# Performance work log

Hardware: AMD Instinct MI355X
Metric: run time of the kernel (lower is better)

The kernel has to match this reference:

```python
import jax, jax.numpy as jnp
import numpy as np

N_NODES = 100000
N_EDGES = 1600000
D_IN = 64
D_OUT = 64
BN_EPS = 1e-5


def setup_inputs() -> dict:
    key = jax.random.key(0)
    ks = jax.random.split(key, 8)
    x = jax.random.normal(ks[0], (N_NODES, D_IN), dtype=jnp.float32)
    edge_index = jax.random.randint(ks[1], (2, N_EDGES), 0, N_NODES, dtype=jnp.int64)
    s_e = 1.0 / np.sqrt(2 * D_IN)
    s_n = 1.0 / np.sqrt(D_IN + D_OUT)
    W_edge = jax.random.uniform(ks[2], (2 * D_IN, D_OUT), jnp.float32, -s_e, s_e)
    b_edge = jax.random.uniform(ks[3], (D_OUT,), jnp.float32, -s_e, s_e)
    W_node = jax.random.uniform(ks[4], (D_IN + D_OUT, D_OUT), jnp.float32, -s_n, s_n)
    b_node = jax.random.uniform(ks[5], (D_OUT,), jnp.float32, -s_n, s_n)
    prelu_a = jnp.asarray(0.25, dtype=jnp.float32)  # nn.PReLU default single slope
    bn_gamma = jnp.ones((D_OUT,), dtype=jnp.float32)
    bn_beta = jnp.zeros((D_OUT,), dtype=jnp.float32)
    return {"x": x, "edge_index": edge_index, "W_edge": W_edge, "b_edge": b_edge,
            "W_node": W_node, "b_node": b_node, "prelu_a": prelu_a,
            "bn_gamma": bn_gamma, "bn_beta": bn_beta}


def reference(x, edge_index, W_edge, b_edge, W_node, b_node, prelu_a, bn_gamma, bn_beta):
    src, dst = edge_index[0], edge_index[1]
    # edge model: message from concat(source, target) node features  [E, 2*D_IN]
    msg_in = jnp.concatenate([x[src], x[dst]], axis=-1)
    msg = msg_in @ W_edge + b_edge                              # [E, D_OUT]
    # scatter-sum aggregate messages at destination nodes       [N, D_OUT]
    agg = jax.ops.segment_sum(msg, dst, num_segments=N_NODES)
    # node model
    h = jnp.concatenate([x, agg], axis=-1) @ W_node + b_node    # [N, D_OUT]
    # PReLU (single shared slope)
    h = jnp.where(h >= 0, h, prelu_a * h)
    # BatchNorm over nodes (training-mode batch stats, biased variance)
    mean = jnp.mean(h, axis=0)
    var = jnp.mean(jnp.square(h - mean), axis=0)
    h = (h - mean) * jax.lax.rsqrt(var + BN_EPS) * bn_gamma + bn_beta
    return h
```

## Files before the change

### kernel.cpp

```cpp
#include <hip/hip_runtime.h>
#include <hip/hip_fp16.h>

typedef _Float16 f16x8 __attribute__((ext_vector_type(8)));
typedef _Float16 f16x2 __attribute__((ext_vector_type(2)));
typedef float f32x4 __attribute__((ext_vector_type(4)));

#define NPB 256
#define FCHUNK 6144
#define MAXBK 512
#define CAPP 5120
#define CAP8 6144

__global__ __launch_bounds__(256) void k_prep(
    const float4* __restrict__ x4, __half2* __restrict__ xh2, int n4, int XGRID,
    const float* __restrict__ We, const float* __restrict__ be,
    const float* __restrict__ Wn, __half* __restrict__ Wfrag, float* __restrict__ c2,
    int* __restrict__ cur, float* __restrict__ stats, int nbuck, int N) {
  int b = blockIdx.x, t = threadIdx.x;
  if (b < XGRID) {
    int i = b * 256 + t;
    if (i < n4) {
      float4 v = x4[i];
      __half2 a, c;
      a.x = __float2half_rn(v.x); a.y = __float2half_rn(v.y);
      c.x = __float2half_rn(v.z); c.y = __float2half_rn(v.w);
      xh2[2 * i] = a;
      xh2[2 * i + 1] = c;
    }
  } else {
    int mb = b - XGRID;
    if (mb < 24) {
      int mat = mb >> 3, kk = (mb >> 2) & 1, ct = mb & 3;
      for (int tt = t; tt < 512; tt += 256) {
        int lane = tt >> 3, j = tt & 7;
        int k = kk * 32 + ((lane >> 4) & 3) * 8 + j;
        int col = ct * 16 + (lane & 15);
        float v;
        if (mat == 0) {
          v = Wn[k * 64 + col];
        } else if (mat == 1) {
          float a = 0.f;
          for (int m = 0; m < 64; ++m) a += We[k * 64 + m] * Wn[(64 + m) * 64 + col];
          v = a;
        } else {
          float a = 0.f;
          for (int m = 0; m < 64; ++m) a += We[(64 + k) * 64 + m] * Wn[(64 + m) * 64 + col];
          v = a;
        }
        Wfrag[mb * 512 + tt] = __float2half_rn(v);
      }
    } else if (mb == 24) {
      if (t < 64) {
        float a = 0.f;
        for (int m = 0; m < 64; ++m) a += be[m] * Wn[(64 + m) * 64 + t];
        c2[t] = a;
      } else if (t < 96) {
        __half2 z; z.x = __float2half_rn(0.f); z.y = __float2half_rn(0.f);
        xh2[(size_t)N * 32 + (t - 64)] = z;
      }
    } else {
      for (int i = t; i < nbuck; i += 256) cur[i] = i * CAPP;
      if (t < 128) stats[t] = 0.f;
    }
  }
}

__global__ __launch_bounds__(1024) void k_fill3(const int* __restrict__ src,
    const int* __restrict__ dst, int* __restrict__ cur,
    int* __restrict__ packed, int E) {
  __shared__ int lh[MAXBK];
  __shared__ int gbase[MAXBK];
  int t = threadIdx.x;
  int e0 = blockIdx.x * FCHUNK;
  int e1 = min(e0 + FCHUNK, E);
  for (int i = t; i < MAXBK; i += 1024) lh[i] = 0;
  __syncthreads();
  int dv[6];
#pragma unroll
  for (int i = 0; i < 6; ++i) {
    int e = e0 + t + i * 1024;
    dv[i] = (e < e1) ? dst[e] : -1;
    if (dv[i] >= 0) atomicAdd(&lh[dv[i] >> 8], 1);
  }
  __syncthreads();
  for (int i = t; i < MAXBK; i += 1024) {
    int c = lh[i];
    gbase[i] = c ? atomicAdd(&cur[i], c) : 0;
    lh[i] = 0;
  }
  __syncthreads();
#pragma unroll
  for (int i = 0; i < 6; ++i) {
    int d = dv[i];
    if (d >= 0) {
      int e = e0 + t + i * 1024;
      int bk = d >> 8;
      int lp = atomicAdd(&lh[bk], 1);
      packed[gbase[bk] + lp] = src[e] | ((d & 255) << 20);
    }
  }
}

__global__ __launch_bounds__(256) void k_sort(const int* __restrict__ packed,
    const int* __restrict__ cur, int* __restrict__ csr,
    int* __restrict__ offA, int* __restrict__ deg, int N) {
  __shared__ int hist[NPB];
  __shared__ int sc[NPB];
  __shared__ int curs[NPB];
  int b = blockIdx.x, t = threadIdx.x;
  hist[t] = 0;
  __syncthreads();
  int e0 = b * CAPP;
  int e1 = cur[b];
  for (int e = e0 + t; e < e1; e += 256)
    atomicAdd(&hist[(packed[e] >> 20) & 255], 1);
  __syncthreads();
  int v = hist[t];
  int pv = (v + 7) & ~7;
  sc[t] = pv;
  __syncthreads();
  for (int d = 1; d < 256; d <<= 1) {
    int a = (t >= d) ? sc[t - d] : 0;
    __syncthreads();
    sc[t] += a;
    __syncthreads();
  }
  int ex = b * CAP8 + sc[t] - pv;
  curs[t] = ex;
  int n = b * NPB + t;
  if (n < N) { offA[n] = ex; deg[n] = v; }
  __syncthreads();
  for (int e = e0 + t; e < e1; e += 256) {
    int pk = packed[e];
    int p = atomicAdd(&curs[(pk >> 20) & 255], 1);
    csr[p] = pk & 0xFFFFF;
  }
  for (int k = v; k < pv; ++k) csr[ex + k] = N;
}

__global__ void k_agg(const f16x2* __restrict__ xh2, const int* __restrict__ offA,
                      const int* __restrict__ deg, const int* __restrict__ csr,
                      f16x2* __restrict__ Sh2, int N) {
  int t = threadIdx.x;
  unsigned lane = t & 63;
  unsigned f = lane & 31;
  int slot = (int)(lane >> 5);
  int wid = (blockIdx.x * blockDim.x + t) >> 6;
  int nw = (gridDim.x * blockDim.x) >> 6;
  for (int n = wid; n < N; n += 2 * nw) {
    int nB = n + nw;
    int j0A = offA[n];
    int pdA = (deg[n] + 7) & ~7;
    int j0B = (nB < N) ? offA[nB] : 0;
    int pdB = (nB < N) ? ((deg[nB] + 7) & ~7) : 0;
    f16x2 aA0 = {0, 0}, aA1 = {0, 0}, aB0 = {0, 0}, aB1 = {0, 0};
    int jA = 0, jB = 0;
    for (; jA < pdA && jB < pdB; jA += 8, jB += 8) {
      int ua = __builtin_amdgcn_readfirstlane(j0A + jA);
      int ub = __builtin_amdgcn_readfirstlane(j0B + jB);
      int a0 = csr[ua + 0], a1 = csr[ua + 1], a2 = csr[ua + 2], a3 = csr[ua + 3];
      int a4 = csr[ua + 4], a5 = csr[ua + 5], a6 = csr[ua + 6], a7 = csr[ua + 7];
      int b0 = csr[ub + 0], b1 = csr[ub + 1], b2 = csr[ub + 2], b3 = csr[ub + 3];
      int b4 = csr[ub + 4], b5 = csr[ub + 5], b6 = csr[ub + 6], b7 = csr[ub + 7];
      unsigned sA0 = (unsigned)(slot ? a1 : a0), sA1 = (unsigned)(slot ? a3 : a2);
      unsigned sA2 = (unsigned)(slot ? a5 : a4), sA3 = (unsigned)(slot ? a7 : a6);
      unsigned sB0 = (unsigned)(slot ? b1 : b0), sB1 = (unsigned)(slot ? b3 : b2);
      unsigned sB2 = (unsigned)(slot ? b5 : b4), sB3 = (unsigned)(slot ? b7 : b6);
      f16x2 vA0 = xh2[(sA0 << 5) | f], vA1 = xh2[(sA1 << 5) | f];
      f16x2 vA2 = xh2[(sA2 << 5) | f], vA3 = xh2[(sA3 << 5) | f];
      f16x2 vB0 = xh2[(sB0 << 5) | f], vB1 = xh2[(sB1 << 5) | f];
      f16x2 vB2 = xh2[(sB2 << 5) | f], vB3 = xh2[(sB3 << 5) | f];
      aA0 += vA0; aA1 += vA1; aA0 += vA2; aA1 += vA3;
      aB0 += vB0; aB1 += vB1; aB0 += vB2; aB1 += vB3;
    }
    for (; jA < pdA; jA += 8) {
      int ua = __builtin_amdgcn_readfirstlane(j0A + jA);
      int a0 = csr[ua + 0], a1 = csr[ua + 1], a2 = csr[ua + 2], a3 = csr[ua + 3];
      int a4 = csr[ua + 4], a5 = csr[ua + 5], a6 = csr[ua + 6], a7 = csr[ua + 7];
      unsigned s0 = (unsigned)(slot ? a1 : a0), s1 = (unsigned)(slot ? a3 : a2);
      unsigned s2 = (unsigned)(slot ? a5 : a4), s3 = (unsigned)(slot ? a7 : a6);
      aA0 += xh2[(s0 << 5) | f]; aA1 += xh2[(s1 << 5) | f];
      aA0 += xh2[(s2 << 5) | f]; aA1 += xh2[(s3 << 5) | f];
    }
    for (; jB < pdB; jB += 8) {
      int ub = __builtin_amdgcn_readfirstlane(j0B + jB);
      int b0 = csr[ub + 0], b1 = csr[ub + 1], b2 = csr[ub + 2], b3 = csr[ub + 3];
      int b4 = csr[ub + 4], b5 = csr[ub + 5], b6 = csr[ub + 6], b7 = csr[ub + 7];
      unsigned s0 = (unsigned)(slot ? b1 : b0), s1 = (unsigned)(slot ? b3 : b2);
      unsigned s2 = (unsigned)(slot ? b5 : b4), s3 = (unsigned)(slot ? b7 : b6);
      aB0 += xh2[(s0 << 5) | f]; aB1 += xh2[(s1 << 5) | f];
      aB0 += xh2[(s2 << 5) | f]; aB1 += xh2[(s3 << 5) | f];
    }
    f16x2 pa = aA0 + aA1;
    unsigned ua = __builtin_bit_cast(unsigned, pa);
    unsigned ux = (unsigned)__shfl_xor((int)ua, 32);
    f16x2 totA = pa + __builtin_bit_cast(f16x2, ux);
    if (slot == 0) Sh2[((unsigned)n << 5) | f] = totA;
    if (nB < N) {
      f16x2 pb = aB0 + aB1;
      unsigned vb = __builtin_bit_cast(unsigned, pb);
      unsigned vx = (unsigned)__shfl_xor((int)vb, 32);
      f16x2 totB = pb + __builtin_bit_cast(f16x2, vx);
      if (slot == 0) Sh2[((unsigned)nB << 5) | f] = totB;
    }
  }
}

__global__ __launch_bounds__(256) void k_nodeM(const __half* __restrict__ xh,
    const __half* __restrict__ Sh, const int* __restrict__ deg,
    const __half* __restrict__ Wfrag, const float* __restrict__ c2,
    const float* __restrict__ bnode, const float* __restrict__ pa,
    __half* __restrict__ Hh, int N) {
  const f16x8* WF = (const f16x8*)Wfrag;
  int t = threadIdx.x, lane = t & 63;
  f16x8 B[24];
#pragma unroll
  for (int f = 0; f < 24; ++f) B[f] = WF[f * 64 + lane];
  float slope = pa[0];
  int wid = (blockIdx.x * blockDim.x + t) >> 6;
  int nw = (gridDim.x * blockDim.x) >> 6;
  int ntile = N >> 4;
  int r = lane & 15, g = lane >> 4;
  for (int tile = wid; tile < ntile; tile += nw) {
    int n0 = tile << 4;
    float dg[4];
#pragma unroll
    for (int q = 0; q < 4; ++q) dg[q] = (float)deg[n0 + g * 4 + q];
    const f16x8* xp = (const f16x8*)(xh + (size_t)(n0 + r) * 64 + g * 8);
    const f16x8* sp = (const f16x8*)(Sh + (size_t)(n0 + r) * 64 + g * 8);
    f16x8 ax0 = xp[0], ax1 = xp[4];
    f16x8 as0 = sp[0], as1 = sp[4];
    f32x4 accA[4], accB[4];
#pragma unroll
    for (int ct = 0; ct < 4; ++ct) {
      f32x4 a = {0.f, 0.f, 0.f, 0.f};
      a = __builtin_amdgcn_mfma_f32_16x16x32_f16(ax0, B[0 + ct], a, 0, 0, 0);
      a = __builtin_amdgcn_mfma_f32_16x16x32_f16(ax1, B[4 + ct], a, 0, 0, 0);
      a = __builtin_amdgcn_mfma_f32_16x16x32_f16(as0, B[8 + ct], a, 0, 0, 0);
      a = __builtin_amdgcn_mfma_f32_16x16x32_f16(as1, B[12 + ct], a, 0, 0, 0);
      accA[ct] = a;
      f32x4 bb = {0.f, 0.f, 0.f, 0.f};
      bb = __builtin_amdgcn_mfma_f32_16x16x32_f16(ax0, B[16 + ct], bb, 0, 0, 0);
      bb = __builtin_amdgcn_mfma_f32_16x16x32_f16(ax1, B[20 + ct], bb, 0, 0, 0);
      accB[ct] = bb;
    }
#pragma unroll
    for (int ct = 0; ct < 4; ++ct) {
      int c = ct * 16 + r;
      float cc = c2[c], bv = bnode[c];
#pragma unroll
      for (int q = 0; q < 4; ++q) {
        float hv = accA[ct][q] + dg[q] * (accB[ct][q] + cc) + bv;
        hv = hv >= 0.f ? hv : slope * hv;
        Hh[(size_t)(n0 + g * 4 + q) * 64 + c] = __float2half_rn(hv);
      }
    }
  }
}

__global__ __launch_bounds__(256) void k_stats(const __half2* __restrict__ hh,
    float* __restrict__ stats, int n2) {
  __shared__ float ls[128];
  int t = threadIdx.x;
  if (t < 128) ls[t] = 0.f;
  __syncthreads();
  int cb = (t & 31) * 2;
  float s0 = 0.f, q0 = 0.f, s1 = 0.f, q1 = 0.f;
  int stride = gridDim.x * 256;
  for (int i = blockIdx.x * 256 + t; i < n2; i += stride) {
    __half2 v = hh[i];
    float a = __half2float(v.x), b = __half2float(v.y);
    s0 += a; q0 += a * a;
    s1 += b; q1 += b * b;
  }
  atomicAdd(&ls[cb], s0);
  atomicAdd(&ls[cb + 1], s1);
  atomicAdd(&ls[64 + cb], q0);
  atomicAdd(&ls[64 + cb + 1], q1);
  __syncthreads();
  if (t < 128) atomicAdd(&stats[t], ls[t]);
}

__global__ void k_out2(const __half2* __restrict__ hh, const float* __restrict__ stats,
                       const float* __restrict__ gamma, const float* __restrict__ beta,
                       float2* __restrict__ out2, int n2, float invN) {
  int i = blockIdx.x * blockDim.x + threadIdx.x;
  if (i < n2) {
    int cb = (i & 31) * 2;
    float m0 = stats[cb] * invN, m1 = stats[cb + 1] * invN;
    float v0 = stats[64 + cb] * invN - m0 * m0;
    float v1 = stats[64 + cb + 1] * invN - m1 * m1;
    float sc0 = gamma[cb] * rsqrtf(v0 + 1e-5f);
    float sc1 = gamma[cb + 1] * rsqrtf(v1 + 1e-5f);
    float sh0 = beta[cb] - m0 * sc0;
    float sh1 = beta[cb + 1] - m1 * sc1;
    __half2 v = hh[i];
    float2 o;
    o.x = __half2float(v.x) * sc0 + sh0;
    o.y = __half2float(v.y) * sc1 + sh1;
    out2[i] = o;
  }
}


extern "C" void kernel_launch(void* const* d_in, const int* in_sizes, int n_in,
                              void* d_out, int out_size, void* d_ws, size_t ws_size,
                              hipStream_t stream) {
  const float* x     = (const float*)d_in[0];
  const int*   ei    = (const int*)d_in[1];
  const float* We    = (const float*)d_in[2];
  const float* be    = (const float*)d_in[3];
  const float* Wn    = (const float*)d_in[4];
  const float* bnode = (const float*)d_in[5];
  const float* pa    = (const float*)d_in[6];
  const float* gamma = (const float*)d_in[7];
  const float* beta  = (const float*)d_in[8];

  int N = in_sizes[0] / 64;
  int E = in_sizes[1] / 2;
  const int* srcA = ei;
  const int* dstA = ei + E;

  int NBUCK = (N + NPB - 1) / NPB;

  char* ws = (char*)d_ws;
  size_t off = 0;
  auto alloc = [&](size_t bytes) -> void* {
    void* p = (void*)(ws + off);
    off += (bytes + 255) & ~(size_t)255;
    return p;
  };
  int*    cur    = (int*)alloc((size_t)NBUCK * 4);
  float*  stats  = (float*)alloc(128 * 4);
  int*    packed = (int*)alloc((size_t)NBUCK * CAPP * 4);
  int*    csr    = (int*)alloc((size_t)NBUCK * CAP8 * 4);
  int*    offA   = (int*)alloc((size_t)N * 4);
  int*    deg    = (int*)alloc((size_t)N * 4);
  __half* xh     = (__half*)alloc((size_t)(N + 1) * 64 * 2);
  __half* Sh     = (__half*)alloc((size_t)N * 64 * 2);
  __half* Hh     = (__half*)alloc((size_t)N * 64 * 2);
  __half* Wfrag  = (__half*)alloc((size_t)24 * 512 * 2);
  float*  c2     = (float*)alloc(64 * 4);

  int FGRID = (E + FCHUNK - 1) / FCHUNK;
  int n4 = N * 16;
  int XGRID = (n4 + 255) / 256;
  int n2 = N * 32;
  int ntile = N / 16;
  int mgrid = (ntile + 3) / 4;

  k_prep<<<XGRID + 26, 256, 0, stream>>>(
      (const float4*)x, (__half2*)xh, n4, XGRID, We, be, Wn, Wfrag, c2,
      cur, stats, NBUCK, N);
  k_fill3<<<FGRID, 1024, 0, stream>>>(srcA, dstA, cur, packed, E);
  k_sort<<<NBUCK, 256, 0, stream>>>(packed, cur, csr, offA, deg, N);
  k_agg<<<2048, 256, 0, stream>>>((const f16x2*)xh, offA, deg, csr, (f16x2*)Sh, N);
  k_nodeM<<<mgrid, 256, 0, stream>>>(xh, Sh, deg, Wfrag, c2, bnode, pa, Hh, N);
  k_stats<<<256, 256, 0, stream>>>((const __half2*)Hh, stats, n2);
  k_out2<<<(n2 + 255) / 256, 256, 0, stream>>>((const __half2*)Hh, stats, gamma, beta,
                                               (float2*)d_out, n2, 1.0f / (float)N);
}
```

Baseline: 128.0 us.

## Fuse BatchNorm stat accumulation into node kernel and widen sort blocks

The node-model kernel now accumulates per-column sum and sum-of-squares of the activations in registers and shared memory, then writes per-block partials. A small kernel reduces those partials, so the separate pass that re-read the whole fp16 H buffer for statistics is gone. Separately, the bucket sort kernel runs 1024 threads per block instead of 256, giving more parallelism on the histogram and scatter loops. Statistics are now taken from fp32 values before fp16 rounding, and the partial buffer adds a little workspace.

```diff
diff --git a/kernel.cpp b/kernel.cpp
--- a/kernel.cpp
+++ b/kernel.cpp
@@ -101,41 +101,43 @@
   }
 }
 
-__global__ __launch_bounds__(256) void k_sort(const int* __restrict__ packed,
+__global__ __launch_bounds__(1024) void k_sort(const int* __restrict__ packed,
     const int* __restrict__ cur, int* __restrict__ csr,
     int* __restrict__ offA, int* __restrict__ deg, int N) {
   __shared__ int hist[NPB];
   __shared__ int sc[NPB];
   __shared__ int curs[NPB];
   int b = blockIdx.x, t = threadIdx.x;
-  hist[t] = 0;
+  if (t < NPB) hist[t] = 0;
   __syncthreads();
   int e0 = b * CAPP;
   int e1 = cur[b];
-  for (int e = e0 + t; e < e1; e += 256)
+  for (int e = e0 + t; e < e1; e += 1024)
     atomicAdd(&hist[(packed[e] >> 20) & 255], 1);
   __syncthreads();
-  int v = hist[t];
+  int v = (t < NPB) ? hist[t] : 0;
   int pv = (v + 7) & ~7;
-  sc[t] = pv;
+  if (t < NPB) sc[t] = pv;
   __syncthreads();
   for (int d = 1; d < 256; d <<= 1) {
-    int a = (t >= d) ? sc[t - d] : 0;
+    int a = (t >= d && t < NPB) ? sc[t - d] : 0;
     __syncthreads();
-    sc[t] += a;
+    if (t < NPB) sc[t] += a;
     __syncthreads();
   }
-  int ex = b * CAP8 + sc[t] - pv;
-  curs[t] = ex;
-  int n = b * NPB + t;
-  if (n < N) { offA[n] = ex; deg[n] = v; }
-  __syncthreads();
-  for (int e = e0 + t; e < e1; e += 256) {
+  if (t < NPB) {
+    int ex = b * CAP8 + sc[t] - pv;
+    curs[t] = ex;
+    int n = b * NPB + t;
+    if (n < N) { offA[n] = ex; deg[n] = v; }
+    for (int k = v; k < pv; ++k) csr[ex + k] = N;
+  }
+  __syncthreads();
+  for (int e = e0 + t; e < e1; e += 1024) {
     int pk = packed[e];
     int p = atomicAdd(&curs[(pk >> 20) & 255], 1);
     csr[p] = pk & 0xFFFFF;
   }
-  for (int k = v; k < pv; ++k) csr[ex + k] = N;
 }
 
 __global__ void k_agg(const f16x2* __restrict__ xh2, const int* __restrict__ offA,
@@ -210,9 +212,11 @@
     const __half* __restrict__ Sh, const int* __restrict__ deg,
     const __half* __restrict__ Wfrag, const float* __restrict__ c2,
     const float* __restrict__ bnode, const float* __restrict__ pa,
-    __half* __restrict__ Hh, int N) {
+    __half* __restrict__ Hh, float* __restrict__ pstats, int N) {
+  __shared__ float ls[128];
   const f16x8* WF = (const f16x8*)Wfrag;
   int t = threadIdx.x, lane = t & 63;
+  if (t < 128) ls[t] = 0.f;
   f16x8 B[24];
 #pragma unroll
   for (int f = 0; f < 24; ++f) B[f] = WF[f * 64 + lane];
@@ -221,6 +225,8 @@
   int nw = (gridDim.x * blockDim.x) >> 6;
   int ntile = N >> 4;
   int r = lane & 15, g = lane >> 4;
+  float ws[4] = {0, 0, 0, 0}, wq[4] = {0, 0, 0, 0};
+  __syncthreads();
   for (int tile = wid; tile < ntile; tile += nw) {
     int n0 = tile << 4;
     float dg[4];
@@ -252,33 +258,30 @@
       for (int q = 0; q < 4; ++q) {
         float hv = accA[ct][q] + dg[q] * (accB[ct][q] + cc) + bv;
         hv = hv >= 0.f ? hv : slope * hv;
+        ws[ct] += hv; wq[ct] += hv * hv;
         Hh[(size_t)(n0 + g * 4 + q) * 64 + c] = __float2half_rn(hv);
       }
     }
   }
-}
-
-__global__ __launch_bounds__(256) void k_stats(const __half2* __restrict__ hh,
-    float* __restrict__ stats, int n2) {
-  __shared__ float ls[128];
+#pragma unroll
+  for (int ct = 0; ct < 4; ++ct) {
+    int c = ct * 16 + r;
+    atomicAdd(&ls[c], ws[ct]);
+    atomicAdd(&ls[64 + c], wq[ct]);
+  }
+  __syncthreads();
+  if (t < 128) pstats[(size_t)blockIdx.x * 128 + t] = ls[t];
+}
+
+__global__ __launch_bounds__(256) void k_stats(const float* __restrict__ pstats,
+    float* __restrict__ stats, int nb) {
   int t = threadIdx.x;
-  if (t < 128) ls[t] = 0.f;
-  __syncthreads();
-  int cb = (t & 31) * 2;
-  float s0 = 0.f, q0 = 0.f, s1 = 0.f, q1 = 0.f;
-  int stride = gridDim.x * 256;
-  for (int i = blockIdx.x * 256 + t; i < n2; i += stride) {
-    __half2 v = hh[i];
-    float a = __half2float(v.x), b = __half2float(v.y);
-    s0 += a; q0 += a * a;
-    s1 += b; q1 += b * b;
-  }
-  atomicAdd(&ls[cb], s0);
-  atomicAdd(&ls[cb + 1], s1);
-  atomicAdd(&ls[64 + cb], q0);
-  atomicAdd(&ls[64 + cb + 1], q1);
-  __syncthreads();
-  if (t < 128) atomicAdd(&stats[t], ls[t]);
+  int col = t & 127;
+  int half = t >> 7;
+  float acc = 0.f;
+  for (int i = blockIdx.x * 2 + half; i < nb; i += gridDim.x * 2)
+    acc += pstats[(size_t)i * 128 + col];
+  atomicAdd(&stats[col], acc);
 }
 
 __global__ void k_out2(const __half2* __restrict__ hh, const float* __restrict__ stats,
@@ -330,6 +333,9 @@
     off += (bytes + 255) & ~(size_t)255;
     return p;
   };
+  int ntile = N / 16;
+  int mgrid = (ntile + 3) / 4;
+
   int*    cur    = (int*)alloc((size_t)NBUCK * 4);
   float*  stats  = (float*)alloc(128 * 4);
   int*    packed = (int*)alloc((size_t)NBUCK * CAPP * 4);
@@ -341,22 +347,21 @@
   __half* Hh     = (__half*)alloc((size_t)N * 64 * 2);
   __half* Wfrag  = (__half*)alloc((size_t)24 * 512 * 2);
   float*  c2     = (float*)alloc(64 * 4);
+  float*  pstats = (float*)alloc((size_t)mgrid * 128 * 4);
 
   int FGRID = (E + FCHUNK - 1) / FCHUNK;
   int n4 = N * 16;
   int XGRID = (n4 + 255) / 256;
   int n2 = N * 32;
-  int ntile = N / 16;
-  int mgrid = (ntile + 3) / 4;
 
   k_prep<<<XGRID + 26, 256, 0, stream>>>(
       (const float4*)x, (__half2*)xh, n4, XGRID, We, be, Wn, Wfrag, c2,
       cur, stats, NBUCK, N);
   k_fill3<<<FGRID, 1024, 0, stream>>>(srcA, dstA, cur, packed, E);
-  k_sort<<<NBUCK, 256, 0, stream>>>(packed, cur, csr, offA, deg, N);
+  k_sort<<<NBUCK, 1024, 0, stream>>>(packed, cur, csr, offA, deg, N);
   k_agg<<<2048, 256, 0, stream>>>((const f16x2*)xh, offA, deg, csr, (f16x2*)Sh, N);
-  k_nodeM<<<mgrid, 256, 0, stream>>>(xh, Sh, deg, Wfrag, c2, bnode, pa, Hh, N);
-  k_stats<<<256, 256, 0, stream>>>((const __half2*)Hh, stats, n2);
+  k_nodeM<<<mgrid, 256, 0, stream>>>(xh, Sh, deg, Wfrag, c2, bnode, pa, Hh, pstats, N);
+  k_stats<<<64, 256, 0, stream>>>(pstats, stats, mgrid);
   k_out2<<<(n2 + 255) / 256, 256, 0, stream>>>((const __half2*)Hh, stats, gamma, beta,
                                                (float2*)d_out, n2, 1.0f / (float)N);
 }
```

Result: no change. 128.2 us (+0.2%).
